# Optimization experiments

Measured on AMD Instinct MI355X. Metric: run time of the kernel, lower is better.

The kernel has to match this reference:

```python
import jax, jax.numpy as jnp
import numpy as np

B, C_IN, H, W = 4, 128, 32, 32
C_SKIP, C_OUT = 64, 64
D_MODEL = 2 * C_SKIP            # 128 (channels after concat)
D_STATE, D_CONV, EXPAND = 16, 4, 2
D_INNER = EXPAND * D_MODEL      # 256
DT_RANK = int(np.ceil(D_MODEL / 16))  # 8
LN_EPS = 1e-5


def setup_inputs() -> dict:
    key = jax.random.key(0)
    ks = jax.random.split(key, 12)
    s = 0.02
    return {
        "x": jax.random.normal(ks[0], (B, C_IN, H, W), jnp.float32),
        "skip_x": jax.random.normal(ks[1], (B, C_SKIP, 2 * H, 2 * W), jnp.float32),
        # ConvTranspose2d(in, skip, k=2, s=2): torch weight layout (in, out, kh, kw)
        "up_w": jax.random.normal(ks[2], (C_IN, C_SKIP, 2, 2), jnp.float32) * s,
        "up_b": jnp.zeros((C_SKIP,), jnp.float32),
        # Mamba params (torch Linear layout: (out_features, in_features))
        "in_proj_w": jax.random.normal(ks[3], (2 * D_INNER, D_MODEL), jnp.float32) * s,
        "conv1d_w": jax.random.normal(ks[4], (D_INNER, 1, D_CONV), jnp.float32) * s,
        "conv1d_b": jnp.zeros((D_INNER,), jnp.float32),
        "x_proj_w": jax.random.normal(ks[5], (DT_RANK + 2 * D_STATE, D_INNER), jnp.float32) * s,
        "dt_proj_w": jax.random.normal(ks[6], (D_INNER, DT_RANK), jnp.float32) * s,
        "dt_proj_b": jnp.zeros((D_INNER,), jnp.float32),
        "A_log": jnp.log(jnp.broadcast_to(jnp.arange(1, D_STATE + 1, dtype=jnp.float32), (D_INNER, D_STATE))),
        "Dp": jnp.ones((D_INNER,), jnp.float32),
        "out_proj_w": jax.random.normal(ks[7], (D_MODEL, D_INNER), jnp.float32) * s,
        "ln_gamma": jnp.ones((D_MODEL,), jnp.float32),
        "ln_beta": jnp.zeros((D_MODEL,), jnp.float32),
        # Conv2d 1x1 (out, in)
        "convout_w": jax.random.normal(ks[8], (C_OUT, D_MODEL), jnp.float32) * s,
        "convout_b": jnp.zeros((C_OUT,), jnp.float32),
    }


def _selective_scan(u, delta, A, Bm, Cm, Dp):
    # u, delta: (B,L,Din); A: (Din,Ds); Bm, Cm: (B,L,Ds)
    deltaA = jnp.exp(delta[..., None] * A)                        # (B,L,Din,Ds)
    deltaBu = delta[..., None] * Bm[:, :, None, :] * u[..., None]  # (B,L,Din,Ds)

    def step(h, xs):
        dA, dBu, c = xs                 # (B,Din,Ds),(B,Din,Ds),(B,Ds)
        h = dA * h + dBu
        y = jnp.einsum('bdn,bn->bd', h, c)
        return h, y

    h0 = jnp.zeros((u.shape[0], D_INNER, D_STATE), u.dtype)
    xs = (deltaA.transpose(1, 0, 2, 3), deltaBu.transpose(1, 0, 2, 3), Cm.transpose(1, 0, 2))
    _, ys = jax.lax.scan(step, h0, xs)  # (L,B,Din)
    return ys.transpose(1, 0, 2) + u * Dp


def _mamba(seq, in_proj_w, conv1d_w, conv1d_b, x_proj_w, dt_proj_w, dt_proj_b, A_log, Dp, out_proj_w):
    # seq: (B, L, D_MODEL)
    xz = seq @ in_proj_w.T                      # (B,L,2*Din)
    u, z = jnp.split(xz, 2, axis=-1)
    # depthwise causal conv1d along L
    uc = u.transpose(0, 2, 1)                   # (B,Din,L)
    uc = jax.lax.conv_general_dilated(
        uc, conv1d_w, window_strides=(1,), padding=[(D_CONV - 1, 0)],
        feature_group_count=D_INNER, dimension_numbers=('NCH', 'OIH', 'NCH'))
    uc = uc + conv1d_b[None, :, None]
    u = jax.nn.silu(uc.transpose(0, 2, 1))      # (B,L,Din)
    dbc = u @ x_proj_w.T                        # (B,L,DT_RANK+2*Ds)
    dt, Bm, Cm = jnp.split(dbc, [DT_RANK, DT_RANK + D_STATE], axis=-1)
    delta = jax.nn.softplus(dt @ dt_proj_w.T + dt_proj_b)
    A = -jnp.exp(A_log)
    y = _selective_scan(u, delta, A, Bm, Cm, Dp)
    y = y * jax.nn.silu(z)
    return y @ out_proj_w.T                     # (B,L,D_MODEL)


def reference(x, skip_x, up_w, up_b, in_proj_w, conv1d_w, conv1d_b, x_proj_w,
              dt_proj_w, dt_proj_b, A_log, Dp, out_proj_w, ln_gamma, ln_beta,
              convout_w, convout_b):
    b, _, h, w = x.shape
    # ConvTranspose2d k=2 s=2: each pixel expands to a 2x2 block
    up = jnp.einsum('bchw,coij->bohiwj', x, up_w).reshape(b, C_SKIP, 2 * h, 2 * w)
    up = up + up_b[None, :, None, None]
    xc = jnp.concatenate([up, skip_x], axis=1)  # (B, D_MODEL, 2H, 2W)
    Hh, Ww = xc.shape[2], xc.shape[3]
    seq = xc.reshape(b, D_MODEL, Hh * Ww).transpose(0, 2, 1)  # (B,L,D)
    y = _mamba(seq, in_proj_w, conv1d_w, conv1d_b, x_proj_w, dt_proj_w,
               dt_proj_b, A_log, Dp, out_proj_w)
    xm = y.transpose(0, 2, 1).reshape(b, D_MODEL, Hh, Ww)
    # permute -> LayerNorm over channels -> permute back
    xn = xm.transpose(0, 2, 3, 1)
    mu = xn.mean(-1, keepdims=True)
    var = xn.var(-1, keepdims=True)
    xn = (xn - mu) * jax.lax.rsqrt(var + LN_EPS) * ln_gamma + ln_beta
    xm = jax.nn.silu(xn.transpose(0, 3, 1, 2))
    out = jnp.einsum('bchw,oc->bohw', xm, convout_w) + convout_b[None, :, None, None]
    return out
```

## Files before the change

kernel.cpp:

```cpp
#include <hip/hip_runtime.h>

#define L_SEQ 4096
#define DM 128
#define DIN 256
#define NC 128
#define CHUNK 32

__global__ __launch_bounds__(256) void upcat_kernel(
    const float* __restrict__ x, const float* __restrict__ skip,
    const float* __restrict__ up_w, const float* __restrict__ up_b,
    float* __restrict__ seq) {
  int b = blockIdx.x >> 6, hh = blockIdx.x & 63;
  int h = hh >> 1, i = hh & 1;
  int tid = threadIdx.x;
  __shared__ float xs[128][32];
  __shared__ float wsh[2][128][64];
  for (int e = tid; e < 1024; e += 256) {
    int c = e >> 3, q = e & 7;
    *(float4*)&xs[c][q * 4] =
        *(const float4*)(x + (((size_t)b * 128 + c) * 32 + h) * 32 + q * 4);
  }
  for (int e = tid; e < 8192; e += 256) {
    int c = e >> 6, o = e & 63;
    float2 v = *(const float2*)(up_w + c * 256 + o * 4 + i * 2);
    wsh[0][c][o] = v.x;
    wsh[1][c][o] = v.y;
  }
  __syncthreads();
  int tx = tid & 15, ty = tid >> 4;
  float4 bv = *(const float4*)(up_b + tx * 4);
  float acc[4][4];
#pragma unroll
  for (int a = 0; a < 4; ++a) {
    acc[a][0] = bv.x; acc[a][1] = bv.y; acc[a][2] = bv.z; acc[a][3] = bv.w;
  }
#pragma unroll 4
  for (int c = 0; c < 128; ++c) {
    float x0 = xs[c][ty * 2];
    float x1 = xs[c][ty * 2 + 1];
    float4 w0 = *(const float4*)&wsh[0][c][tx * 4];
    float4 w1 = *(const float4*)&wsh[1][c][tx * 4];
    acc[0][0] = fmaf(x0, w0.x, acc[0][0]); acc[0][1] = fmaf(x0, w0.y, acc[0][1]);
    acc[0][2] = fmaf(x0, w0.z, acc[0][2]); acc[0][3] = fmaf(x0, w0.w, acc[0][3]);
    acc[1][0] = fmaf(x0, w1.x, acc[1][0]); acc[1][1] = fmaf(x0, w1.y, acc[1][1]);
    acc[1][2] = fmaf(x0, w1.z, acc[1][2]); acc[1][3] = fmaf(x0, w1.w, acc[1][3]);
    acc[2][0] = fmaf(x1, w0.x, acc[2][0]); acc[2][1] = fmaf(x1, w0.y, acc[2][1]);
    acc[2][2] = fmaf(x1, w0.z, acc[2][2]); acc[2][3] = fmaf(x1, w0.w, acc[2][3]);
    acc[3][0] = fmaf(x1, w1.x, acc[3][0]); acc[3][1] = fmaf(x1, w1.y, acc[3][1]);
    acc[3][2] = fmaf(x1, w1.z, acc[3][2]); acc[3][3] = fmaf(x1, w1.w, acc[3][3]);
  }
  size_t mrow_base = (size_t)b * L_SEQ + (size_t)hh * 64;
#pragma unroll
  for (int a = 0; a < 4; ++a) {
    int ww = ty * 4 + a;
    *(float4*)(seq + (mrow_base + ww) * DM + tx * 4) =
        make_float4(acc[a][0], acc[a][1], acc[a][2], acc[a][3]);
  }
  for (int e = tid; e < 4096; e += 256) {
    int c = e & 63, ww = e >> 6;
    seq[(mrow_base + ww) * DM + 64 + c] =
        skip[((size_t)b * 64 + c) * (size_t)L_SEQ + hh * 64 + ww];
  }
}

__global__ __launch_bounds__(256) void gemm_bt(
    const float* __restrict__ A, const float* __restrict__ W,
    float* __restrict__ C, int M, int N, int K) {
  __shared__ float As[32][68];
  __shared__ float Ws[32][68];
  int m0 = blockIdx.x * 64, n0 = blockIdx.y * 64;
  int tid = threadIdx.x;
  int tx = tid & 15, ty = tid >> 4;
  float acc[4][4];
#pragma unroll
  for (int a = 0; a < 4; ++a)
#pragma unroll
    for (int bb = 0; bb < 4; ++bb) acc[a][bb] = 0.f;

  for (int k0 = 0; k0 < K; k0 += 32) {
    __syncthreads();
    for (int e = tid; e < 512; e += 256) {
      int r = e >> 3;
      int c4 = (e & 7) << 2;
      float4 va = *(const float4*)(A + (size_t)(m0 + r) * K + k0 + c4);
      As[c4 + 0][r] = va.x; As[c4 + 1][r] = va.y;
      As[c4 + 2][r] = va.z; As[c4 + 3][r] = va.w;
      float4 vw = *(const float4*)(W + (size_t)(n0 + r) * K + k0 + c4);
      Ws[c4 + 0][r] = vw.x; Ws[c4 + 1][r] = vw.y;
      Ws[c4 + 2][r] = vw.z; Ws[c4 + 3][r] = vw.w;
    }
    __syncthreads();
#pragma unroll
    for (int kk = 0; kk < 32; ++kk) {
      float4 av = *(const float4*)(&As[kk][ty * 4]);
      float4 wv = *(const float4*)(&Ws[kk][tx * 4]);
      float av_[4] = {av.x, av.y, av.z, av.w};
      float wv_[4] = {wv.x, wv.y, wv.z, wv.w};
#pragma unroll
      for (int a = 0; a < 4; ++a)
#pragma unroll
        for (int bb = 0; bb < 4; ++bb)
          acc[a][bb] = fmaf(av_[a], wv_[bb], acc[a][bb]);
    }
  }
#pragma unroll
  for (int a = 0; a < 4; ++a)
#pragma unroll
    for (int bb = 0; bb < 4; ++bb)
      C[(size_t)(m0 + ty * 4 + a) * N + n0 + tx * 4 + bb] = acc[a][bb];
}

__global__ __launch_bounds__(256) void conv_silu_kernel(
    const float* __restrict__ xz, const float* __restrict__ cw,
    const float* __restrict__ cb, float* __restrict__ u) {
  int idx = blockIdx.x * 256 + threadIdx.x;
  int d = idx & 255;
  int m = idx >> 8;
  int l = m & (L_SEQ - 1);
  float acc = cb[d];
#pragma unroll
  for (int t = 0; t < 4; ++t) {
    int ls = l - 3 + t;
    if (ls >= 0)
      acc = fmaf(xz[(size_t)(m - 3 + t) * 512 + d], cw[d * 4 + t], acc);
  }
  u[idx] = acc / (1.f + __expf(-acc));
}

__global__ __launch_bounds__(256) void xproj_kernel(
    const float* __restrict__ u, const float* __restrict__ W,
    float* __restrict__ dbc) {
  __shared__ float us[64][68];
  int m0 = blockIdx.x * 64;
  int tid = threadIdx.x;
  int lane = tid & 63;
  int w = __builtin_amdgcn_readfirstlane(tid >> 6);
  const float* Wb = W + w * 10 * 256;
  float acc[10];
#pragma unroll
  for (int j = 0; j < 10; ++j) acc[j] = 0.f;
  for (int k0 = 0; k0 < 256; k0 += 64) {
    __syncthreads();
    for (int e = tid; e < 1024; e += 256) {
      int r = e >> 4, q = e & 15;
      float4 v = *(const float4*)(u + (size_t)(m0 + r) * 256 + k0 + q * 4);
      *(float4*)&us[r][q * 4] = v;
    }
    __syncthreads();
#pragma unroll
    for (int kk = 0; kk < 64; kk += 4) {
      float4 a4 = *(const float4*)&us[lane][kk];
      float a_[4] = {a4.x, a4.y, a4.z, a4.w};
#pragma unroll
      for (int i = 0; i < 4; ++i)
#pragma unroll
        for (int j = 0; j < 10; ++j)
          acc[j] = fmaf(a_[i], Wb[j * 256 + k0 + kk + i], acc[j]);
    }
  }
  size_t base = (size_t)(m0 + lane) * 40 + w * 10;
#pragma unroll
  for (int j = 0; j < 10; ++j) dbc[base + j] = acc[j];
}


__device__ __forceinline__ float softplus_f(float a) {
  return (a > 20.f) ? a : log1pf(__expf(a));
}

__global__ __launch_bounds__(256) void scan_pass1(
    const float* __restrict__ u, const float* __restrict__ dbc,
    const float* __restrict__ A_log, const float* __restrict__ Wdt,
    const float* __restrict__ bdt, float* __restrict__ carryA,
    float* __restrict__ carryH) {
  int bid = blockIdx.x;
  int b = bid >> 7;
  int c = bid & (NC - 1);
  int d = threadIdx.x;
  float Ac[16];
  {
    const float4* ar = (const float4*)(A_log + d * 16);
#pragma unroll
    for (int q = 0; q < 4; ++q) {
      float4 v = ar[q];
      Ac[q * 4 + 0] = -__expf(v.x); Ac[q * 4 + 1] = -__expf(v.y);
      Ac[q * 4 + 2] = -__expf(v.z); Ac[q * 4 + 3] = -__expf(v.w);
    }
  }
  float wdt[8];
  {
    const float4* wr = (const float4*)(Wdt + d * 8);
    float4 v0 = wr[0], v1 = wr[1];
    wdt[0] = v0.x; wdt[1] = v0.y; wdt[2] = v0.z; wdt[3] = v0.w;
    wdt[4] = v1.x; wdt[5] = v1.y; wdt[6] = v1.z; wdt[7] = v1.w;
  }
  float bdt_v = bdt[d];
  float h[16], Ap[16];
#pragma unroll
  for (int n = 0; n < 16; ++n) { h[n] = 0.f; Ap[n] = 1.f; }
  size_t l0 = (size_t)b * L_SEQ + (size_t)c * CHUNK;
  const float* up = u + l0 * 256 + d;
  const float* rp = dbc + l0 * 40;
  for (int li = 0; li < CHUNK; ++li) {
    float acc = bdt_v;
#pragma unroll
    for (int j = 0; j < 8; ++j)
      acc = fmaf(rp[li * 40 + j], wdt[j], acc);
    float dv = softplus_f(acc);
    float uv = up[(size_t)li * 256];
    float t = dv * uv;
#pragma unroll
    for (int n = 0; n < 16; ++n) {
      float dA = __expf(dv * Ac[n]);
      h[n] = fmaf(dA, h[n], t * rp[li * 40 + 8 + n]);
      Ap[n] *= dA;
    }
  }
  float4* cA = (float4*)(carryA + ((size_t)bid * 256 + d) * 16);
  float4* cH = (float4*)(carryH + ((size_t)bid * 256 + d) * 16);
#pragma unroll
  for (int q = 0; q < 4; ++q) {
    cA[q] = make_float4(Ap[q * 4], Ap[q * 4 + 1], Ap[q * 4 + 2], Ap[q * 4 + 3]);
    cH[q] = make_float4(h[q * 4], h[q * 4 + 1], h[q * 4 + 2], h[q * 4 + 3]);
  }
}

__global__ __launch_bounds__(256) void scan_mid(
    const float* __restrict__ carryA, float* __restrict__ carryH) {
  int gid = blockIdx.x * 256 + threadIdx.x;
  int b = gid >> 12;
  int dn = gid & 4095;
  float h = 0.f;
  for (int c = 0; c < NC; ++c) {
    size_t i = ((size_t)(b * NC + c) << 12) + dn;
    float a = carryA[i];
    float hl = carryH[i];
    carryH[i] = h;
    h = fmaf(a, h, hl);
  }
}

__global__ __launch_bounds__(256) void scan_pass3(
    const float* __restrict__ u, const float* __restrict__ dbc,
    const float* __restrict__ xz, const float* __restrict__ A_log,
    const float* __restrict__ Wdt, const float* __restrict__ bdt,
    const float* __restrict__ Dp, const float* __restrict__ carryH,
    float* __restrict__ y) {
  int bid = blockIdx.x;
  int b = bid >> 7;
  int c = bid & (NC - 1);
  int d = threadIdx.x;
  float Ac[16];
  {
    const float4* ar = (const float4*)(A_log + d * 16);
#pragma unroll
    for (int q = 0; q < 4; ++q) {
      float4 v = ar[q];
      Ac[q * 4 + 0] = -__expf(v.x); Ac[q * 4 + 1] = -__expf(v.y);
      Ac[q * 4 + 2] = -__expf(v.z); Ac[q * 4 + 3] = -__expf(v.w);
    }
  }
  float wdt[8];
  {
    const float4* wr = (const float4*)(Wdt + d * 8);
    float4 v0 = wr[0], v1 = wr[1];
    wdt[0] = v0.x; wdt[1] = v0.y; wdt[2] = v0.z; wdt[3] = v0.w;
    wdt[4] = v1.x; wdt[5] = v1.y; wdt[6] = v1.z; wdt[7] = v1.w;
  }
  float bdt_v = bdt[d];
  float Dv = Dp[d];
  float h[16];
  {
    const float4* cH = (const float4*)(carryH + ((size_t)bid * 256 + d) * 16);
#pragma unroll
    for (int q = 0; q < 4; ++q) {
      float4 v = cH[q];
      h[q * 4 + 0] = v.x; h[q * 4 + 1] = v.y;
      h[q * 4 + 2] = v.z; h[q * 4 + 3] = v.w;
    }
  }
  size_t l0 = (size_t)b * L_SEQ + (size_t)c * CHUNK;
  const float* up = u + l0 * 256 + d;
  const float* zp = xz + l0 * 512 + 256 + d;
  const float* rp = dbc + l0 * 40;
  float* yp = y + l0 * 256 + d;
  for (int li = 0; li < CHUNK; ++li) {
    float acc = bdt_v;
#pragma unroll
    for (int j = 0; j < 8; ++j)
      acc = fmaf(rp[li * 40 + j], wdt[j], acc);
    float dv = softplus_f(acc);
    float uv = up[(size_t)li * 256];
    float zv = zp[(size_t)li * 512];
    float t = dv * uv;
    float p = 0.f;
#pragma unroll
    for (int n = 0; n < 16; ++n) {
      float dA = __expf(dv * Ac[n]);
      h[n] = fmaf(dA, h[n], t * rp[li * 40 + 8 + n]);
      p = fmaf(h[n], rp[li * 40 + 24 + n], p);
    }
    float s = zv / (1.f + __expf(-zv));
    yp[(size_t)li * 256] = (p + uv * Dv) * s;
  }
}

__global__ __launch_bounds__(256) void ln_out_kernel(
    const float* __restrict__ s2, const float* __restrict__ gamma,
    const float* __restrict__ beta, const float* __restrict__ Wo,
    const float* __restrict__ bo, float* __restrict__ out) {
  __shared__ float xt[64][129];
  __shared__ float mus[64], invs[64];
  int tid = threadIdx.x;
  int m0 = blockIdx.x * 64;
  for (int i = 0; i < 8; ++i) {
    int s = tid + i * 256;
    int r = s >> 5, q = s & 31;
    float4 v = *(const float4*)(s2 + (size_t)(m0 + r) * 128 + q * 4);
    xt[r][q * 4 + 0] = v.x; xt[r][q * 4 + 1] = v.y;
    xt[r][q * 4 + 2] = v.z; xt[r][q * 4 + 3] = v.w;
  }
  __syncthreads();
  {
    int r = tid >> 2, kq = (tid & 3) * 32;
    float s = 0.f, q = 0.f;
#pragma unroll 8
    for (int kk = 0; kk < 32; ++kk) {
      float v = xt[r][kq + kk];
      s += v; q = fmaf(v, v, q);
    }
    s += __shfl_xor(s, 1, 64); s += __shfl_xor(s, 2, 64);
    q += __shfl_xor(q, 1, 64); q += __shfl_xor(q, 2, 64);
    if ((tid & 3) == 0) {
      float mu = s * (1.f / 128.f);
      float var = q * (1.f / 128.f) - mu * mu;
      mus[r] = mu;
      invs[r] = rsqrtf(var + 1e-5f);
    }
  }
  __syncthreads();
  for (int i = 0; i < 32; ++i) {
    int idx = tid + i * 256;
    int r = idx >> 7, k = idx & 127;
    float v = xt[r][k];
    float xn = (v - mus[r]) * invs[r] * gamma[k] + beta[k];
    xt[r][k] = xn / (1.f + __expf(-xn));
  }
  __syncthreads();
  int lane = tid & 63;
  int w = __builtin_amdgcn_readfirstlane(tid >> 6);
  int cbase = blockIdx.y * 32 + w * 8;
  const float* Wrow = Wo + cbase * 128;
  float acc[8];
#pragma unroll
  for (int j = 0; j < 8; ++j) acc[j] = 0.f;
#pragma unroll 4
  for (int k = 0; k < 128; ++k) {
    float v = xt[lane][k];
#pragma unroll
    for (int j = 0; j < 8; ++j)
      acc[j] = fmaf(v, Wrow[j * 128 + k], acc[j]);
  }
  int m = m0 + lane;
  int b = m >> 12, l = m & 4095;
#pragma unroll
  for (int j = 0; j < 8; ++j)
    out[((size_t)b * 64 + cbase + j) * 4096 + l] = acc[j] + bo[cbase + j];
}

extern "C" void kernel_launch(void* const* d_in, const int* in_sizes, int n_in,
                              void* d_out, int out_size, void* d_ws, size_t ws_size,
                              hipStream_t stream) {
  (void)in_sizes; (void)n_in; (void)out_size; (void)ws_size;
  const float* x         = (const float*)d_in[0];
  const float* skip      = (const float*)d_in[1];
  const float* up_w      = (const float*)d_in[2];
  const float* up_b      = (const float*)d_in[3];
  const float* in_proj_w = (const float*)d_in[4];
  const float* conv1d_w  = (const float*)d_in[5];
  const float* conv1d_b  = (const float*)d_in[6];
  const float* x_proj_w  = (const float*)d_in[7];
  const float* dt_proj_w = (const float*)d_in[8];
  const float* dt_proj_b = (const float*)d_in[9];
  const float* A_log     = (const float*)d_in[10];
  const float* Dp        = (const float*)d_in[11];
  const float* out_proj_w= (const float*)d_in[12];
  const float* ln_gamma  = (const float*)d_in[13];
  const float* ln_beta   = (const float*)d_in[14];
  const float* convout_w = (const float*)d_in[15];
  const float* convout_b = (const float*)d_in[16];
  float* out = (float*)d_out;
  float* ws  = (float*)d_ws;

  float* seq    = ws;
  float* xz     = ws + 2097152;
  float* u      = ws + 10485760;
  float* dbc    = ws + 14680064;
  float* y      = ws + 15335424;
  float* carryA = ws + 19529728;
  float* carryH = ws + 21626880;

  upcat_kernel<<<256, 256, 0, stream>>>(x, skip, up_w, up_b, seq);
  gemm_bt<<<dim3(16384 / 64, 512 / 64), 256, 0, stream>>>(seq, in_proj_w, xz,
                                                          16384, 512, 128);
  conv_silu_kernel<<<16384, 256, 0, stream>>>(xz, conv1d_w, conv1d_b, u);
  xproj_kernel<<<16384 / 64, 256, 0, stream>>>(u, x_proj_w, dbc);
  scan_pass1<<<4 * NC, 256, 0, stream>>>(u, dbc, A_log, dt_proj_w, dt_proj_b,
                                         carryA, carryH);
  scan_mid<<<64, 256, 0, stream>>>(carryA, carryH);
  scan_pass3<<<4 * NC, 256, 0, stream>>>(u, dbc, xz, A_log, dt_proj_w,
                                         dt_proj_b, Dp, carryH, y);
  gemm_bt<<<dim3(16384 / 64, 128 / 64), 256, 0, stream>>>(y, out_proj_w, seq,
                                                          16384, 128, 256);
  ln_out_kernel<<<dim3(256, 2), 256, 0, stream>>>(seq, ln_gamma, ln_beta,
                                                  convout_w, convout_b, out);
}
```

Before: 237.0 us.

## Stage dbc chunk in LDS, prefetch u/z into registers, compute carryA from delta sum

Both scan passes now copy each chunk's 32x40 dt/B/C rows into shared memory once per block, and preload the per-thread u (and z) column values for the whole chunk into registers before the unrolled time loop. Pass 1 no longer multiplies a running product of per-step decays; it accumulates the sum of delta and takes one exp of sum*A at the end, which is algebraically equal. This is meant to cut redundant broadcast global loads and serialized load latency inside the sequential loop, and to remove 16 multiplies per step. The cost is much higher register pressure from the 32- or 64-entry register arrays plus the full unroll, which may lower occupancy.

```diff
diff --git a/kernel.cpp b/kernel.cpp
--- a/kernel.cpp
+++ b/kernel.cpp
@@ -177,6 +177,10 @@
   int b = bid >> 7;
   int c = bid & (NC - 1);
   int d = threadIdx.x;
+  __shared__ float ls[CHUNK * 40];
+  size_t l0 = (size_t)b * L_SEQ + (size_t)c * CHUNK;
+  const float* rp = dbc + l0 * 40;
+  for (int e = d; e < CHUNK * 40; e += 256) ls[e] = rp[e];
   float Ac[16];
   {
     const float4* ar = (const float4*)(A_log + d * 16);
@@ -195,32 +199,36 @@
     wdt[4] = v1.x; wdt[5] = v1.y; wdt[6] = v1.z; wdt[7] = v1.w;
   }
   float bdt_v = bdt[d];
-  float h[16], Ap[16];
-#pragma unroll
-  for (int n = 0; n < 16; ++n) { h[n] = 0.f; Ap[n] = 1.f; }
-  size_t l0 = (size_t)b * L_SEQ + (size_t)c * CHUNK;
+  float ur[CHUNK];
   const float* up = u + l0 * 256 + d;
-  const float* rp = dbc + l0 * 40;
+#pragma unroll
+  for (int li = 0; li < CHUNK; ++li) ur[li] = up[(size_t)li * 256];
+  __syncthreads();
+  float h[16];
+#pragma unroll
+  for (int n = 0; n < 16; ++n) h[n] = 0.f;
+  float dvs = 0.f;
+#pragma unroll
   for (int li = 0; li < CHUNK; ++li) {
     float acc = bdt_v;
 #pragma unroll
     for (int j = 0; j < 8; ++j)
-      acc = fmaf(rp[li * 40 + j], wdt[j], acc);
+      acc = fmaf(ls[li * 40 + j], wdt[j], acc);
     float dv = softplus_f(acc);
-    float uv = up[(size_t)li * 256];
-    float t = dv * uv;
+    dvs += dv;
+    float t = dv * ur[li];
 #pragma unroll
     for (int n = 0; n < 16; ++n) {
       float dA = __expf(dv * Ac[n]);
-      h[n] = fmaf(dA, h[n], t * rp[li * 40 + 8 + n]);
-      Ap[n] *= dA;
+      h[n] = fmaf(dA, h[n], t * ls[li * 40 + 8 + n]);
     }
   }
   float4* cA = (float4*)(carryA + ((size_t)bid * 256 + d) * 16);
   float4* cH = (float4*)(carryH + ((size_t)bid * 256 + d) * 16);
 #pragma unroll
   for (int q = 0; q < 4; ++q) {
-    cA[q] = make_float4(Ap[q * 4], Ap[q * 4 + 1], Ap[q * 4 + 2], Ap[q * 4 + 3]);
+    cA[q] = make_float4(__expf(dvs * Ac[q * 4]), __expf(dvs * Ac[q * 4 + 1]),
+                        __expf(dvs * Ac[q * 4 + 2]), __expf(dvs * Ac[q * 4 + 3]));
     cH[q] = make_float4(h[q * 4], h[q * 4 + 1], h[q * 4 + 2], h[q * 4 + 3]);
   }
 }
@@ -250,6 +258,10 @@
   int b = bid >> 7;
   int c = bid & (NC - 1);
   int d = threadIdx.x;
+  __shared__ float ls[CHUNK * 40];
+  size_t l0 = (size_t)b * L_SEQ + (size_t)c * CHUNK;
+  const float* rp = dbc + l0 * 40;
+  for (int e = d; e < CHUNK * 40; e += 256) ls[e] = rp[e];
   float Ac[16];
   {
     const float4* ar = (const float4*)(A_log + d * 16);
@@ -269,6 +281,13 @@
   }
   float bdt_v = bdt[d];
   float Dv = Dp[d];
+  float ur[CHUNK], zr[CHUNK];
+  const float* up = u + l0 * 256 + d;
+  const float* zp = xz + l0 * 512 + 256 + d;
+#pragma unroll
+  for (int li = 0; li < CHUNK; ++li) ur[li] = up[(size_t)li * 256];
+#pragma unroll
+  for (int li = 0; li < CHUNK; ++li) zr[li] = zp[(size_t)li * 512];
   float h[16];
   {
     const float4* cH = (const float4*)(carryH + ((size_t)bid * 256 + d) * 16);
@@ -279,26 +298,24 @@
       h[q * 4 + 2] = v.z; h[q * 4 + 3] = v.w;
     }
   }
-  size_t l0 = (size_t)b * L_SEQ + (size_t)c * CHUNK;
-  const float* up = u + l0 * 256 + d;
-  const float* zp = xz + l0 * 512 + 256 + d;
-  const float* rp = dbc + l0 * 40;
+  __syncthreads();
   float* yp = y + l0 * 256 + d;
+#pragma unroll
   for (int li = 0; li < CHUNK; ++li) {
     float acc = bdt_v;
 #pragma unroll
     for (int j = 0; j < 8; ++j)
-      acc = fmaf(rp[li * 40 + j], wdt[j], acc);
+      acc = fmaf(ls[li * 40 + j], wdt[j], acc);
     float dv = softplus_f(acc);
-    float uv = up[(size_t)li * 256];
-    float zv = zp[(size_t)li * 512];
+    float uv = ur[li];
+    float zv = zr[li];
     float t = dv * uv;
     float p = 0.f;
 #pragma unroll
     for (int n = 0; n < 16; ++n) {
       float dA = __expf(dv * Ac[n]);
-      h[n] = fmaf(dA, h[n], t * rp[li * 40 + 8 + n]);
-      p = fmaf(h[n], rp[li * 40 + 24 + n], p);
+      h[n] = fmaf(dA, h[n], t * ls[li * 40 + 8 + n]);
+      p = fmaf(h[n], ls[li * 40 + 24 + n], p);
     }
     float s = zv / (1.f + __expf(-zv));
     yp[(size_t)li * 256] = (p + uv * Dv) * s;
```

Result: slower. 248.5 us (+4.9%).
